# Kernel tuning notes

Measured on AMD Instinct MI355X. Metric: run time of the kernel, lower is better.

## Reference

```python
import jax, jax.numpy as jnp
import numpy as np

HIDDEN = 512
INPUT = 512
BATCH = 16384


def _quant_dequant(w):
    # mirrors torch: scale = max(|w|)/127 + 1e-8; int8 round-clamp; dequantize
    scale = jnp.max(jnp.abs(w)) / 127.0 + 1e-8
    q = jnp.clip(jnp.round(w / scale), -128, 127)
    return q * scale


def setup_inputs() -> dict:
    key = jax.random.key(0)
    ks = jax.random.split(key, 7)
    x = jax.random.normal(ks[0], (BATCH, INPUT), dtype=jnp.float32)
    h_prev = jax.random.normal(ks[1], (BATCH, HIDDEN), dtype=jnp.float32)
    c_prev = jax.random.normal(ks[2], (BATCH, HIDDEN), dtype=jnp.float32)
    w_ih = _quant_dequant(jax.random.normal(ks[3], (4 * HIDDEN, INPUT), dtype=jnp.float32) * 0.05)
    w_hh = _quant_dequant(jax.random.normal(ks[4], (4 * HIDDEN, HIDDEN), dtype=jnp.float32) * 0.05)
    bias_ih = jax.random.normal(ks[5], (4 * HIDDEN,), dtype=jnp.float32) * 0.05
    bias_hh = jax.random.normal(ks[6], (4 * HIDDEN,), dtype=jnp.float32) * 0.05
    return {"x": x, "h_prev": h_prev, "c_prev": c_prev,
            "w_ih": w_ih, "w_hh": w_hh, "bias_ih": bias_ih, "bias_hh": bias_hh}


def reference(x, h_prev, c_prev, w_ih, w_hh, bias_ih, bias_hh):
    # gates: [B, 4H]
    gates = x @ w_ih.T + bias_ih + h_prev @ w_hh.T + bias_hh
    i_g, f_g, g_g, o_g = jnp.split(gates, 4, axis=1)
    i_g = jax.nn.sigmoid(i_g)
    f_g = jax.nn.sigmoid(f_g)
    g_g = jnp.tanh(g_g)
    o_g = jax.nn.sigmoid(o_g)
    c_new = f_g * c_prev + i_g * g_g
    h_new = o_g * jnp.tanh(c_new)
    return (h_new, c_new)
```

## Files before the change

kernel.cpp:

```cpp
#include <hip/hip_runtime.h>


typedef __attribute__((ext_vector_type(8))) short short8;
typedef __attribute__((ext_vector_type(4))) float f32x4;
typedef unsigned int u32;
typedef unsigned short u16;

#define BATCH 16384
#define HID 512
#define KTOT 1024
#define BM 128
#define BK 64
#define KSTEPS 16
#define TILE_BYTES 16384
#define WSA_BYTES (128ull * KSTEPS * TILE_BYTES)
#define WSW_BYTES (16ull * KSTEPS * TILE_BYTES)
#define WS_NEEDED (WSA_BYTES + WSW_BYTES)

__device__ __forceinline__ u16 f2bf(float f) {
    u32 u = __builtin_bit_cast(u32, f);
    u += 0x7FFFu + ((u >> 16) & 1u);
    return (u16)(u >> 16);
}

__device__ __forceinline__ float sigmoidf_(float v) { return 1.0f / (1.0f + __expf(-v)); }
__device__ __forceinline__ float tanhf_(float v) { return 1.0f - 2.0f / (__expf(2.0f * v) + 1.0f); }

__device__ __forceinline__ void gload_lds16(const void* g, void* l) {
    __builtin_amdgcn_global_load_lds(
        (const __attribute__((address_space(1))) u32*)g,
        (__attribute__((address_space(3))) u32*)l, 16, 0, 0);
}

__global__ __launch_bounds__(256) void pack_a(
    const float* __restrict__ x, const float* __restrict__ h_prev, u16* __restrict__ wsA)
{
    const u32 idx = blockIdx.x * 256 + threadIdx.x;
    const u32 cphys = idx & 7;
    const u32 row = (idx >> 3) & 127;
    const u32 ks = (idx >> 10) & 15;
    const u32 bm = idx >> 14;
    const u32 clog = cphys ^ (row & 7);
    const u32 m = bm * 128 + row;
    const u32 kglob = ks * 64 + clog * 8;
    const float* src = (kglob < 512) ? (x + (size_t)m * 512 + kglob)
                                     : (h_prev + (size_t)m * 512 + (kglob - 512));
    const float4 v0 = *(const float4*)src;
    const float4 v1 = *(const float4*)(src + 4);
    ushort4 p0, p1;
    p0.x = f2bf(v0.x); p0.y = f2bf(v0.y); p0.z = f2bf(v0.z); p0.w = f2bf(v0.w);
    p1.x = f2bf(v1.x); p1.y = f2bf(v1.y); p1.z = f2bf(v1.z); p1.w = f2bf(v1.w);
    *(ushort4*)(wsA + (size_t)idx * 8) = p0;
    *(ushort4*)(wsA + (size_t)idx * 8 + 4) = p1;
}

__global__ __launch_bounds__(256) void pack_w(
    const float* __restrict__ w_ih, const float* __restrict__ w_hh, u16* __restrict__ wsW)
{
    const u32 idx = blockIdx.x * 256 + threadIdx.x;
    const u32 cphys = idx & 7;
    const u32 row = (idx >> 3) & 127;
    const u32 ks = (idx >> 10) & 15;
    const u32 bn = idx >> 14;
    const u32 clog = cphys ^ (row & 7);
    const u32 g = row >> 5, rr = row & 31;
    const u32 wrow = g * 512 + bn * 32 + rr;
    const u32 kglob = ks * 64 + clog * 8;
    const float* src = (kglob < 512) ? (w_ih + (size_t)wrow * 512 + kglob)
                                     : (w_hh + (size_t)wrow * 512 + (kglob - 512));
    const float4 v0 = *(const float4*)src;
    const float4 v1 = *(const float4*)(src + 4);
    ushort4 p0, p1;
    p0.x = f2bf(v0.x); p0.y = f2bf(v0.y); p0.z = f2bf(v0.z); p0.w = f2bf(v0.w);
    p1.x = f2bf(v1.x); p1.y = f2bf(v1.y); p1.z = f2bf(v1.z); p1.w = f2bf(v1.w);
    *(ushort4*)(wsW + (size_t)idx * 8) = p0;
    *(ushort4*)(wsW + (size_t)idx * 8 + 4) = p1;
}

__global__ __launch_bounds__(256, 4) void lstm_gemm(
    const u16* __restrict__ wsA, const u16* __restrict__ wsW,
    const float* __restrict__ c_prev,
    const float* __restrict__ b_ih, const float* __restrict__ b_hh,
    float* __restrict__ h_out, float* __restrict__ c_out)
{
    __shared__ u16 sA[BM * BK];
    __shared__ u16 sW[BM * BK];

    const int t = threadIdx.x;
    const int bn = blockIdx.x & 15;
    const int bm = blockIdx.x >> 4;
    const int n0 = bn * 32;
    const int rowBase = bm * BM;

    const int lane = t & 63;
    const int wv = t >> 6;
    const int colin = lane & 15;
    const int quad = lane >> 4;
    const int stageOff = wv * 1024 + lane * 16;

    f32x4 acc[2][2][4];
    #pragma unroll
    for (int rf = 0; rf < 2; ++rf)
        #pragma unroll
        for (int cc = 0; cc < 2; ++cc)
            #pragma unroll
            for (int g = 0; g < 4; ++g)
                acc[rf][cc][g] = (f32x4){0.f, 0.f, 0.f, 0.f};

    const char* gA = (const char*)wsA + (size_t)bm * KSTEPS * TILE_BYTES;
    const char* gW = (const char*)wsW + (size_t)bn * KSTEPS * TILE_BYTES;

    for (int ks = 0; ks < KSTEPS; ++ks) {
        __syncthreads();
        #pragma unroll
        for (int j = 0; j < 4; ++j) {
            const int off = j * 4096 + stageOff;
            gload_lds16(gA + (size_t)ks * TILE_BYTES + off, (char*)sA + off);
            gload_lds16(gW + (size_t)ks * TILE_BYTES + off, (char*)sW + off);
        }
        __syncthreads();

        #pragma unroll
        for (int ks2 = 0; ks2 < 2; ++ks2) {
            short8 af[2];
            #pragma unroll
            for (int rf = 0; rf < 2; ++rf) {
                const int row = wv * 32 + rf * 16 + colin;
                const int boff = row * 128 + (((ks2 * 4 + quad) ^ (row & 7)) * 16);
                af[rf] = *(const short8*)((const char*)sA + boff);
            }
            short8 bfr[2][4];
            #pragma unroll
            for (int cc = 0; cc < 2; ++cc)
                #pragma unroll
                for (int g = 0; g < 4; ++g) {
                    const int row = g * 32 + cc * 16 + colin;
                    const int boff = row * 128 + (((ks2 * 4 + quad) ^ (row & 7)) * 16);
                    bfr[cc][g] = *(const short8*)((const char*)sW + boff);
                }
            #pragma unroll
            for (int rf = 0; rf < 2; ++rf)
                #pragma unroll
                for (int cc = 0; cc < 2; ++cc)
                    #pragma unroll
                    for (int g = 0; g < 4; ++g)
                        acc[rf][cc][g] = __builtin_amdgcn_mfma_f32_16x16x32_bf16(
                            af[rf], bfr[cc][g], acc[rf][cc][g], 0, 0, 0);
        }
    }

    float bsum[2][4];
    #pragma unroll
    for (int cc = 0; cc < 2; ++cc) {
        const int colg = n0 + cc * 16 + colin;
        #pragma unroll
        for (int g = 0; g < 4; ++g)
            bsum[cc][g] = b_ih[g * 512 + colg] + b_hh[g * 512 + colg];
    }

    #pragma unroll
    for (int rf = 0; rf < 2; ++rf)
        #pragma unroll
        for (int cc = 0; cc < 2; ++cc) {
            const int colg = n0 + cc * 16 + colin;
            #pragma unroll
            for (int reg = 0; reg < 4; ++reg) {
                const int row = rowBase + wv * 32 + rf * 16 + quad * 4 + reg;
                const size_t off = (size_t)row * 512 + colg;
                const float ig = acc[rf][cc][0][reg] + bsum[cc][0];
                const float fg = acc[rf][cc][1][reg] + bsum[cc][1];
                const float gg = acc[rf][cc][2][reg] + bsum[cc][2];
                const float og = acc[rf][cc][3][reg] + bsum[cc][3];
                const float cp = c_prev[off];
                const float cn = sigmoidf_(fg) * cp + sigmoidf_(ig) * tanhf_(gg);
                const float hn = sigmoidf_(og) * tanhf_(cn);
                h_out[off] = hn;
                c_out[off] = cn;
            }
        }
}

#define LDSK 72
__global__ __launch_bounds__(256, 3) void lstm_fused_v1(
    const float* __restrict__ x, const float* __restrict__ h_prev,
    const float* __restrict__ c_prev, const float* __restrict__ w_ih,
    const float* __restrict__ w_hh, const float* __restrict__ b_ih,
    const float* __restrict__ b_hh, float* __restrict__ h_out,
    float* __restrict__ c_out)
{
    __shared__ u16 sA[BM][LDSK];
    __shared__ u16 sW[BM][LDSK];
    const int t = threadIdx.x;
    const int bn = blockIdx.x & 15, bm = blockIdx.x >> 4;
    const int n0 = bn * 32, rowBase = bm * BM;
    const int srow = t >> 4, scol = t & 15;
    const int lane = t & 63, wv = t >> 6, colin = lane & 15, quad = lane >> 4;
    f32x4 acc[2][2][4];
    #pragma unroll
    for (int rf = 0; rf < 2; ++rf)
        #pragma unroll
        for (int cc = 0; cc < 2; ++cc)
            #pragma unroll
            for (int g = 0; g < 4; ++g) acc[rf][cc][g] = (f32x4){0.f, 0.f, 0.f, 0.f};
    for (int k0 = 0; k0 < KTOT; k0 += BK) {
        const int kk = (k0 < 512) ? k0 : (k0 - 512);
        const float* aSrc = (k0 < 512) ? x : h_prev;
        const float* wSrc = (k0 < 512) ? w_ih : w_hh;
        __syncthreads();
        #pragma unroll
        for (int p = 0; p < 8; ++p) {
            const int r = srow + p * 16;
            const float4 av = *(const float4*)(aSrc + (size_t)(rowBase + r) * 512 + kk + scol * 4);
            ushort4 ap; ap.x = f2bf(av.x); ap.y = f2bf(av.y); ap.z = f2bf(av.z); ap.w = f2bf(av.w);
            *(ushort4*)&sA[r][scol * 4] = ap;
            const int gate = r >> 5, rr = r & 31;
            const float4 wvv = *(const float4*)(wSrc + (size_t)(gate * 512 + n0 + rr) * 512 + kk + scol * 4);
            ushort4 wp; wp.x = f2bf(wvv.x); wp.y = f2bf(wvv.y); wp.z = f2bf(wvv.z); wp.w = f2bf(wvv.w);
            *(ushort4*)&sW[r][scol * 4] = wp;
        }
        __syncthreads();
        #pragma unroll
        for (int ks = 0; ks < 2; ++ks) {
            short8 af[2];
            #pragma unroll
            for (int rf = 0; rf < 2; ++rf)
                af[rf] = *(const short8*)&sA[wv * 32 + rf * 16 + colin][ks * 32 + quad * 8];
            short8 bfr[2][4];
            #pragma unroll
            for (int cc = 0; cc < 2; ++cc)
                #pragma unroll
                for (int g = 0; g < 4; ++g)
                    bfr[cc][g] = *(const short8*)&sW[g * 32 + cc * 16 + colin][ks * 32 + quad * 8];
            #pragma unroll
            for (int rf = 0; rf < 2; ++rf)
                #pragma unroll
                for (int cc = 0; cc < 2; ++cc)
                    #pragma unroll
                    for (int g = 0; g < 4; ++g)
                        acc[rf][cc][g] = __builtin_amdgcn_mfma_f32_16x16x32_bf16(
                            af[rf], bfr[cc][g], acc[rf][cc][g], 0, 0, 0);
        }
    }
    float bsum[2][4];
    #pragma unroll
    for (int cc = 0; cc < 2; ++cc) {
        const int colg = n0 + cc * 16 + colin;
        #pragma unroll
        for (int g = 0; g < 4; ++g) bsum[cc][g] = b_ih[g * 512 + colg] + b_hh[g * 512 + colg];
    }
    #pragma unroll
    for (int rf = 0; rf < 2; ++rf)
        #pragma unroll
        for (int cc = 0; cc < 2; ++cc) {
            const int colg = n0 + cc * 16 + colin;
            #pragma unroll
            for (int reg = 0; reg < 4; ++reg) {
                const int row = rowBase + wv * 32 + rf * 16 + quad * 4 + reg;
                const size_t off = (size_t)row * 512 + colg;
                const float ig = acc[rf][cc][0][reg] + bsum[cc][0];
                const float fg = acc[rf][cc][1][reg] + bsum[cc][1];
                const float gg = acc[rf][cc][2][reg] + bsum[cc][2];
                const float og = acc[rf][cc][3][reg] + bsum[cc][3];
                const float cp = c_prev[off];
                const float cn = sigmoidf_(fg) * cp + sigmoidf_(ig) * tanhf_(gg);
                const float hn = sigmoidf_(og) * tanhf_(cn);
                h_out[off] = hn;
                c_out[off] = cn;
            }
        }
}

extern "C" void kernel_launch(void* const* d_in, const int* in_sizes, int n_in,
                              void* d_out, int out_size, void* d_ws, size_t ws_size,
                              hipStream_t stream) {
    const float* x      = (const float*)d_in[0];
    const float* h_prev = (const float*)d_in[1];
    const float* c_prev = (const float*)d_in[2];
    const float* w_ih   = (const float*)d_in[3];
    const float* w_hh   = (const float*)d_in[4];
    const float* b_ih   = (const float*)d_in[5];
    const float* b_hh   = (const float*)d_in[6];
    float* h_out = (float*)d_out;
    float* c_out = h_out + (size_t)BATCH * HID;
    const int grid = (BATCH / BM) * (HID / 32);

    if (ws_size >= WS_NEEDED) {
        u16* wsA = (u16*)d_ws;
        u16* wsW = (u16*)((char*)d_ws + WSA_BYTES);
        pack_a<<<(WSA_BYTES / 16) / 256, 256, 0, stream>>>(x, h_prev, wsA);
        pack_w<<<(WSW_BYTES / 16) / 256, 256, 0, stream>>>(w_ih, w_hh, wsW);
        lstm_gemm<<<grid, 256, 0, stream>>>(wsA, wsW, c_prev, b_ih, b_hh, h_out, c_out);
    } else {
        lstm_fused_v1<<<grid, 256, 0, stream>>>(x, h_prev, c_prev, w_ih, w_hh, b_ih, b_hh, h_out, c_out);
    }
}
```

Baseline: 242.0 us.

## Double GEMM M-tile to 256 rows, merge pack kernels, use nontemporal epilogue IO

Each GEMM block now covers 256 batch rows instead of 128, so every wave computes 64 rows and each staged weight tile is reused twice as much. This halves redundant weight loads from L2. The two bf16 pack kernels are merged into one launch to cut launch overhead, and the epilogue reads c_prev and writes h and c with nontemporal hints. In exchange, the bigger accumulator array and LDS footprint lower occupancy to 2 blocks per CU, and the grid drops to 1024 blocks.

```diff
diff --git a/kernel.cpp b/kernel.cpp
--- a/kernel.cpp
+++ b/kernel.cpp
@@ -9,13 +9,18 @@
 #define BATCH 16384
 #define HID 512
 #define KTOT 1024
-#define BM 128
+#define BM 256
 #define BK 64
 #define KSTEPS 16
-#define TILE_BYTES 16384
-#define WSA_BYTES (128ull * KSTEPS * TILE_BYTES)
-#define WSW_BYTES (16ull * KSTEPS * TILE_BYTES)
+#define TILEA_BYTES 32768
+#define TILEW_BYTES 16384
+#define NBM 64
+#define NBN 16
+#define WSA_BYTES ((size_t)NBM * KSTEPS * TILEA_BYTES)
+#define WSW_BYTES ((size_t)NBN * KSTEPS * TILEW_BYTES)
 #define WS_NEEDED (WSA_BYTES + WSW_BYTES)
+#define A_CHUNKS (1u << 21)
+#define W_CHUNKS (1u << 18)
 
 __device__ __forceinline__ u16 f2bf(float f) {
     u32 u = __builtin_bit_cast(u32, f);
@@ -32,59 +37,56 @@
         (__attribute__((address_space(3))) u32*)l, 16, 0, 0);
 }
 
-__global__ __launch_bounds__(256) void pack_a(
-    const float* __restrict__ x, const float* __restrict__ h_prev, u16* __restrict__ wsA)
+__global__ __launch_bounds__(256) void pack_all(
+    const float* __restrict__ x, const float* __restrict__ h_prev,
+    const float* __restrict__ w_ih, const float* __restrict__ w_hh,
+    u16* __restrict__ wsA, u16* __restrict__ wsW)
 {
     const u32 idx = blockIdx.x * 256 + threadIdx.x;
-    const u32 cphys = idx & 7;
-    const u32 row = (idx >> 3) & 127;
-    const u32 ks = (idx >> 10) & 15;
-    const u32 bm = idx >> 14;
-    const u32 clog = cphys ^ (row & 7);
-    const u32 m = bm * 128 + row;
-    const u32 kglob = ks * 64 + clog * 8;
-    const float* src = (kglob < 512) ? (x + (size_t)m * 512 + kglob)
-                                     : (h_prev + (size_t)m * 512 + (kglob - 512));
+    const float* src;
+    u16* dst;
+    if (idx < A_CHUNKS) {
+        const u32 cphys = idx & 7;
+        const u32 row = (idx >> 3) & 255;
+        const u32 ks = (idx >> 11) & 15;
+        const u32 bm = idx >> 15;
+        const u32 clog = cphys ^ (row & 7);
+        const u32 m = bm * 256 + row;
+        const u32 kglob = ks * 64 + clog * 8;
+        src = (kglob < 512) ? (x + (size_t)m * 512 + kglob)
+                            : (h_prev + (size_t)m * 512 + (kglob - 512));
+        dst = wsA + (size_t)idx * 8;
+    } else {
+        const u32 widx = idx - A_CHUNKS;
+        const u32 cphys = widx & 7;
+        const u32 row = (widx >> 3) & 127;
+        const u32 ks = (widx >> 10) & 15;
+        const u32 bn = widx >> 14;
+        const u32 clog = cphys ^ (row & 7);
+        const u32 g = row >> 5, rr = row & 31;
+        const u32 wrow = g * 512 + bn * 32 + rr;
+        const u32 kglob = ks * 64 + clog * 8;
+        src = (kglob < 512) ? (w_ih + (size_t)wrow * 512 + kglob)
+                            : (w_hh + (size_t)wrow * 512 + (kglob - 512));
+        dst = wsW + (size_t)widx * 8;
+    }
     const float4 v0 = *(const float4*)src;
     const float4 v1 = *(const float4*)(src + 4);
     ushort4 p0, p1;
     p0.x = f2bf(v0.x); p0.y = f2bf(v0.y); p0.z = f2bf(v0.z); p0.w = f2bf(v0.w);
     p1.x = f2bf(v1.x); p1.y = f2bf(v1.y); p1.z = f2bf(v1.z); p1.w = f2bf(v1.w);
-    *(ushort4*)(wsA + (size_t)idx * 8) = p0;
-    *(ushort4*)(wsA + (size_t)idx * 8 + 4) = p1;
-}
-
-__global__ __launch_bounds__(256) void pack_w(
-    const float* __restrict__ w_ih, const float* __restrict__ w_hh, u16* __restrict__ wsW)
-{
-    const u32 idx = blockIdx.x * 256 + threadIdx.x;
-    const u32 cphys = idx & 7;
-    const u32 row = (idx >> 3) & 127;
-    const u32 ks = (idx >> 10) & 15;
-    const u32 bn = idx >> 14;
-    const u32 clog = cphys ^ (row & 7);
-    const u32 g = row >> 5, rr = row & 31;
-    const u32 wrow = g * 512 + bn * 32 + rr;
-    const u32 kglob = ks * 64 + clog * 8;
-    const float* src = (kglob < 512) ? (w_ih + (size_t)wrow * 512 + kglob)
-                                     : (w_hh + (size_t)wrow * 512 + (kglob - 512));
-    const float4 v0 = *(const float4*)src;
-    const float4 v1 = *(const float4*)(src + 4);
-    ushort4 p0, p1;
-    p0.x = f2bf(v0.x); p0.y = f2bf(v0.y); p0.z = f2bf(v0.z); p0.w = f2bf(v0.w);
-    p1.x = f2bf(v1.x); p1.y = f2bf(v1.y); p1.z = f2bf(v1.z); p1.w = f2bf(v1.w);
-    *(ushort4*)(wsW + (size_t)idx * 8) = p0;
-    *(ushort4*)(wsW + (size_t)idx * 8 + 4) = p1;
-}
-
-__global__ __launch_bounds__(256, 4) void lstm_gemm(
+    *(ushort4*)dst = p0;
+    *(ushort4*)(dst + 4) = p1;
+}
+
+__global__ __launch_bounds__(256, 2) void lstm_gemm(
     const u16* __restrict__ wsA, const u16* __restrict__ wsW,
     const float* __restrict__ c_prev,
     const float* __restrict__ b_ih, const float* __restrict__ b_hh,
     float* __restrict__ h_out, float* __restrict__ c_out)
 {
     __shared__ u16 sA[BM * BK];
-    __shared__ u16 sW[BM * BK];
+    __shared__ u16 sW[128 * BK];
 
     const int t = threadIdx.x;
     const int bn = blockIdx.x & 15;
@@ -96,36 +98,39 @@
     const int wv = t >> 6;
     const int colin = lane & 15;
     const int quad = lane >> 4;
-    const int stageOff = wv * 1024 + lane * 16;
-
-    f32x4 acc[2][2][4];
-    #pragma unroll
-    for (int rf = 0; rf < 2; ++rf)
+
+    f32x4 acc[4][2][4];
+    #pragma unroll
+    for (int rf = 0; rf < 4; ++rf)
         #pragma unroll
         for (int cc = 0; cc < 2; ++cc)
             #pragma unroll
             for (int g = 0; g < 4; ++g)
                 acc[rf][cc][g] = (f32x4){0.f, 0.f, 0.f, 0.f};
 
-    const char* gA = (const char*)wsA + (size_t)bm * KSTEPS * TILE_BYTES;
-    const char* gW = (const char*)wsW + (size_t)bn * KSTEPS * TILE_BYTES;
-
+    const char* gA = (const char*)wsA + (size_t)bm * KSTEPS * TILEA_BYTES;
+    const char* gW = (const char*)wsW + (size_t)bn * KSTEPS * TILEW_BYTES;
+    const int stageOff = t * 16;
+
+    #pragma unroll 1
     for (int ks = 0; ks < KSTEPS; ++ks) {
         __syncthreads();
         #pragma unroll
-        for (int j = 0; j < 4; ++j) {
-            const int off = j * 4096 + stageOff;
-            gload_lds16(gA + (size_t)ks * TILE_BYTES + off, (char*)sA + off);
-            gload_lds16(gW + (size_t)ks * TILE_BYTES + off, (char*)sW + off);
-        }
+        for (int j = 0; j < 8; ++j)
+            gload_lds16(gA + (size_t)ks * TILEA_BYTES + j * 4096 + stageOff,
+                        (char*)sA + j * 4096 + stageOff);
+        #pragma unroll
+        for (int j = 0; j < 4; ++j)
+            gload_lds16(gW + (size_t)ks * TILEW_BYTES + j * 4096 + stageOff,
+                        (char*)sW + j * 4096 + stageOff);
         __syncthreads();
 
         #pragma unroll
         for (int ks2 = 0; ks2 < 2; ++ks2) {
-            short8 af[2];
-            #pragma unroll
-            for (int rf = 0; rf < 2; ++rf) {
-                const int row = wv * 32 + rf * 16 + colin;
+            short8 af[4];
+            #pragma unroll
+            for (int rf = 0; rf < 4; ++rf) {
+                const int row = wv * 64 + rf * 16 + colin;
                 const int boff = row * 128 + (((ks2 * 4 + quad) ^ (row & 7)) * 16);
                 af[rf] = *(const short8*)((const char*)sA + boff);
             }
@@ -134,12 +139,12 @@
             for (int cc = 0; cc < 2; ++cc)
                 #pragma unroll
                 for (int g = 0; g < 4; ++g) {
-                    const int row = g * 32 + cc * 16 + colin;
-                    const int boff = row * 128 + (((ks2 * 4 + quad) ^ (row & 7)) * 16);
+                    const int wrow = g * 32 + cc * 16 + colin;
+                    const int boff = wrow * 128 + (((ks2 * 4 + quad) ^ (wrow & 7)) * 16);
                     bfr[cc][g] = *(const short8*)((const char*)sW + boff);
                 }
             #pragma unroll
-            for (int rf = 0; rf < 2; ++rf)
+            for (int rf = 0; rf < 4; ++rf)
                 #pragma unroll
                 for (int cc = 0; cc < 2; ++cc)
                     #pragma unroll
@@ -158,6 +163,96 @@
             bsum[cc][g] = b_ih[g * 512 + colg] + b_hh[g * 512 + colg];
     }
 
+    #pragma unroll
+    for (int rf = 0; rf < 4; ++rf)
+        #pragma unroll
+        for (int cc = 0; cc < 2; ++cc) {
+            const int colg = n0 + cc * 16 + colin;
+            #pragma unroll
+            for (int reg = 0; reg < 4; ++reg) {
+                const int row = rowBase + wv * 64 + rf * 16 + quad * 4 + reg;
+                const size_t off = (size_t)row * 512 + colg;
+                const float ig = acc[rf][cc][0][reg] + bsum[cc][0];
+                const float fg = acc[rf][cc][1][reg] + bsum[cc][1];
+                const float gg = acc[rf][cc][2][reg] + bsum[cc][2];
+                const float og = acc[rf][cc][3][reg] + bsum[cc][3];
+                const float cp = __builtin_nontemporal_load(c_prev + off);
+                const float cn = sigmoidf_(fg) * cp + sigmoidf_(ig) * tanhf_(gg);
+                const float hn = sigmoidf_(og) * tanhf_(cn);
+                __builtin_nontemporal_store(hn, h_out + off);
+                __builtin_nontemporal_store(cn, c_out + off);
+            }
+        }
+}
+
+#define LDSK 72
+__global__ __launch_bounds__(256, 3) void lstm_fused_v1(
+    const float* __restrict__ x, const float* __restrict__ h_prev,
+    const float* __restrict__ c_prev, const float* __restrict__ w_ih,
+    const float* __restrict__ w_hh, const float* __restrict__ b_ih,
+    const float* __restrict__ b_hh, float* __restrict__ h_out,
+    float* __restrict__ c_out)
+{
+    __shared__ u16 sA[128][LDSK];
+    __shared__ u16 sW[128][LDSK];
+    const int t = threadIdx.x;
+    const int bn = blockIdx.x & 15, bm = blockIdx.x >> 4;
+    const int n0 = bn * 32, rowBase = bm * 128;
+    const int srow = t >> 4, scol = t & 15;
+    const int lane = t & 63, wv = t >> 6, colin = lane & 15, quad = lane >> 4;
+    f32x4 acc[2][2][4];
+    #pragma unroll
+    for (int rf = 0; rf < 2; ++rf)
+        #pragma unroll
+        for (int cc = 0; cc < 2; ++cc)
+            #pragma unroll
+            for (int g = 0; g < 4; ++g) acc[rf][cc][g] = (f32x4){0.f, 0.f, 0.f, 0.f};
+    for (int k0 = 0; k0 < KTOT; k0 += 64) {
+        const int kk = (k0 < 512) ? k0 : (k0 - 512);
+        const float* aSrc = (k0 < 512) ? x : h_prev;
+        const float* wSrc = (k0 < 512) ? w_ih : w_hh;
+        __syncthreads();
+        #pragma unroll
+        for (int p = 0; p < 8; ++p) {
+            const int r = srow + p * 16;
+            const float4 av = *(const float4*)(aSrc + (size_t)(rowBase + r) * 512 + kk + scol * 4);
+            ushort4 ap; ap.x = f2bf(av.x); ap.y = f2bf(av.y); ap.z = f2bf(av.z); ap.w = f2bf(av.w);
+            *(ushort4*)&sA[r][scol * 4] = ap;
+            const int gate = r >> 5, rr = r & 31;
+            const float4 wvv = *(const float4*)(wSrc + (size_t)(gate * 512 + n0 + rr) * 512 + kk + scol * 4);
+            ushort4 wp; wp.x = f2bf(wvv.x); wp.y = f2bf(wvv.y); wp.z = f2bf(wvv.z); wp.w = f2bf(wvv.w);
+            *(ushort4*)&sW[r][scol * 4] = wp;
+        }
+        __syncthreads();
+        #pragma unroll
+        for (int ks = 0; ks < 2; ++ks) {
+            short8 af[2];
+            #pragma unroll
+            for (int rf = 0; rf < 2; ++rf)
+                af[rf] = *(const short8*)&sA[wv * 32 + rf * 16 + colin][ks * 32 + quad * 8];
+            short8 bfr[2][4];
+            #pragma unroll
+            for (int cc = 0; cc < 2; ++cc)
+                #pragma unroll
+                for (int g = 0; g < 4; ++g)
+                    bfr[cc][g] = *(const short8*)&sW[g * 32 + cc * 16 + colin][ks * 32 + quad * 8];
+            #pragma unroll
+            for (int rf = 0; rf < 2; ++rf)
+                #pragma unroll
+                for (int cc = 0; cc < 2; ++cc)
+                    #pragma unroll
+                    for (int g = 0; g < 4; ++g)
+                        acc[rf][cc][g] = __builtin_amdgcn_mfma_f32_16x16x32_bf16(
+                            af[rf], bfr[cc][g], acc[rf][cc][g], 0, 0, 0);
+        }
+    }
+    float bsum[2][4];
+    #pragma unroll
+    for (int cc = 0; cc < 2; ++cc) {
+        const int colg = n0 + cc * 16 + colin;
+        #pragma unroll
+        for (int g = 0; g < 4; ++g) bsum[cc][g] = b_ih[g * 512 + colg] + b_hh[g * 512 + colg];
+    }
     #pragma unroll
     for (int rf = 0; rf < 2; ++rf)
         #pragma unroll
@@ -180,96 +275,6 @@
         }
 }
 
-#define LDSK 72
-__global__ __launch_bounds__(256, 3) void lstm_fused_v1(
-    const float* __restrict__ x, const float* __restrict__ h_prev,
-    const float* __restrict__ c_prev, const float* __restrict__ w_ih,
-    const float* __restrict__ w_hh, const float* __restrict__ b_ih,
-    const float* __restrict__ b_hh, float* __restrict__ h_out,
-    float* __restrict__ c_out)
-{
-    __shared__ u16 sA[BM][LDSK];
-    __shared__ u16 sW[BM][LDSK];
-    const int t = threadIdx.x;
-    const int bn = blockIdx.x & 15, bm = blockIdx.x >> 4;
-    const int n0 = bn * 32, rowBase = bm * BM;
-    const int srow = t >> 4, scol = t & 15;
-    const int lane = t & 63, wv = t >> 6, colin = lane & 15, quad = lane >> 4;
-    f32x4 acc[2][2][4];
-    #pragma unroll
-    for (int rf = 0; rf < 2; ++rf)
-        #pragma unroll
-        for (int cc = 0; cc < 2; ++cc)
-            #pragma unroll
-            for (int g = 0; g < 4; ++g) acc[rf][cc][g] = (f32x4){0.f, 0.f, 0.f, 0.f};
-    for (int k0 = 0; k0 < KTOT; k0 += BK) {
-        const int kk = (k0 < 512) ? k0 : (k0 - 512);
-        const float* aSrc = (k0 < 512) ? x : h_prev;
-        const float* wSrc = (k0 < 512) ? w_ih : w_hh;
-        __syncthreads();
-        #pragma unroll
-        for (int p = 0; p < 8; ++p) {
-            const int r = srow + p * 16;
-            const float4 av = *(const float4*)(aSrc + (size_t)(rowBase + r) * 512 + kk + scol * 4);
-            ushort4 ap; ap.x = f2bf(av.x); ap.y = f2bf(av.y); ap.z = f2bf(av.z); ap.w = f2bf(av.w);
-            *(ushort4*)&sA[r][scol * 4] = ap;
-            const int gate = r >> 5, rr = r & 31;
-            const float4 wvv = *(const float4*)(wSrc + (size_t)(gate * 512 + n0 + rr) * 512 + kk + scol * 4);
-            ushort4 wp; wp.x = f2bf(wvv.x); wp.y = f2bf(wvv.y); wp.z = f2bf(wvv.z); wp.w = f2bf(wvv.w);
-            *(ushort4*)&sW[r][scol * 4] = wp;
-        }
-        __syncthreads();
-        #pragma unroll
-        for (int ks = 0; ks < 2; ++ks) {
-            short8 af[2];
-            #pragma unroll
-            for (int rf = 0; rf < 2; ++rf)
-                af[rf] = *(const short8*)&sA[wv * 32 + rf * 16 + colin][ks * 32 + quad * 8];
-            short8 bfr[2][4];
-            #pragma unroll
-            for (int cc = 0; cc < 2; ++cc)
-                #pragma unroll
-                for (int g = 0; g < 4; ++g)
-                    bfr[cc][g] = *(const short8*)&sW[g * 32 + cc * 16 + colin][ks * 32 + quad * 8];
-            #pragma unroll
-            for (int rf = 0; rf < 2; ++rf)
-                #pragma unroll
-                for (int cc = 0; cc < 2; ++cc)
-                    #pragma unroll
-                    for (int g = 0; g < 4; ++g)
-                        acc[rf][cc][g] = __builtin_amdgcn_mfma_f32_16x16x32_bf16(
-                            af[rf], bfr[cc][g], acc[rf][cc][g], 0, 0, 0);
-        }
-    }
-    float bsum[2][4];
-    #pragma unroll
-    for (int cc = 0; cc < 2; ++cc) {
-        const int colg = n0 + cc * 16 + colin;
-        #pragma unroll
-        for (int g = 0; g < 4; ++g) bsum[cc][g] = b_ih[g * 512 + colg] + b_hh[g * 512 + colg];
-    }
-    #pragma unroll
-    for (int rf = 0; rf < 2; ++rf)
-        #pragma unroll
-        for (int cc = 0; cc < 2; ++cc) {
-            const int colg = n0 + cc * 16 + colin;
-            #pragma unroll
-            for (int reg = 0; reg < 4; ++reg) {
-                const int row = rowBase + wv * 32 + rf * 16 + quad * 4 + reg;
-                const size_t off = (size_t)row * 512 + colg;
-                const float ig = acc[rf][cc][0][reg] + bsum[cc][0];
-                const float fg = acc[rf][cc][1][reg] + bsum[cc][1];
-                const float gg = acc[rf][cc][2][reg] + bsum[cc][2];
-                const float og = acc[rf][cc][3][reg] + bsum[cc][3];
-                const float cp = c_prev[off];
-                const float cn = sigmoidf_(fg) * cp + sigmoidf_(ig) * tanhf_(gg);
-                const float hn = sigmoidf_(og) * tanhf_(cn);
-                h_out[off] = hn;
-                c_out[off] = cn;
-            }
-        }
-}
-
 extern "C" void kernel_launch(void* const* d_in, const int* in_sizes, int n_in,
                               void* d_out, int out_size, void* d_ws, size_t ws_size,
                               hipStream_t stream) {
@@ -282,15 +287,13 @@
     const float* b_hh   = (const float*)d_in[6];
     float* h_out = (float*)d_out;
     float* c_out = h_out + (size_t)BATCH * HID;
-    const int grid = (BATCH / BM) * (HID / 32);
 
     if (ws_size >= WS_NEEDED) {
         u16* wsA = (u16*)d_ws;
         u16* wsW = (u16*)((char*)d_ws + WSA_BYTES);
-        pack_a<<<(WSA_BYTES / 16) / 256, 256, 0, stream>>>(x, h_prev, wsA);
-        pack_w<<<(WSW_BYTES / 16) / 256, 256, 0, stream>>>(w_ih, w_hh, wsW);
-        lstm_gemm<<<grid, 256, 0, stream>>>(wsA, wsW, c_prev, b_ih, b_hh, h_out, c_out);
+        pack_all<<<(A_CHUNKS + W_CHUNKS) / 256, 256, 0, stream>>>(x, h_prev, w_ih, w_hh, wsA, wsW);
+        lstm_gemm<<<NBM * NBN, 256, 0, stream>>>(wsA, wsW, c_prev, b_ih, b_hh, h_out, c_out);
     } else {
-        lstm_fused_v1<<<grid, 256, 0, stream>>>(x, h_prev, c_prev, w_ih, w_hh, b_ih, b_hh, h_out, c_out);
-    }
-}
+        lstm_fused_v1<<<128 * 16, 256, 0, stream>>>(x, h_prev, c_prev, w_ih, w_hh, b_ih, b_hh, h_out, c_out);
+    }
+}
```

Measured after the change: 233.7 us. 1.04x faster.
